# Kernel tuning notes

Hardware: AMD Instinct MI355X
Metric: run time of the kernel (lower is better)

The kernel has to match this reference:

```python
import jax, jax.numpy as jnp
import numpy as np

N = 50000   # nodes
E = 1000000 # edges
D = 64      # input_dim
H = 64      # hidden dim (both hidden layers)
O = 16      # output_dim
G = 512     # number of graphs in the batch


def setup_inputs() -> dict:
    key = jax.random.key(0)
    ks = jax.random.split(key, 12)
    s = 0.05
    x = jax.random.normal(ks[0], (N, D), dtype=jnp.float32)
    edge_index = jax.random.randint(ks[1], (2, E), 0, N, dtype=jnp.int32)
    batch = jnp.sort(jax.random.randint(ks[2], (N,), 0, G, dtype=jnp.int32))
    # SAGEConv layer 1: lin_l (neighbor aggregate, with bias), lin_r (root, no bias)
    Wl1 = jax.random.normal(ks[3], (D, H), dtype=jnp.float32) * s
    Wr1 = jax.random.normal(ks[4], (D, H), dtype=jnp.float32) * s
    b1 = jnp.zeros((H,), dtype=jnp.float32)
    # SAGEConv layer 2
    Wl2 = jax.random.normal(ks[5], (H, H), dtype=jnp.float32) * s
    Wr2 = jax.random.normal(ks[6], (H, H), dtype=jnp.float32) * s
    b2 = jnp.zeros((H,), dtype=jnp.float32)
    # final Linear head
    Wo = jax.random.normal(ks[7], (H, O), dtype=jnp.float32) * s
    bo = jnp.zeros((O,), dtype=jnp.float32)
    return {"x": x, "edge_index": edge_index, "batch": batch,
            "Wl1": Wl1, "Wr1": Wr1, "b1": b1,
            "Wl2": Wl2, "Wr2": Wr2, "b2": b2,
            "Wo": Wo, "bo": bo}


def reference(x, edge_index, batch, Wl1, Wr1, b1, Wl2, Wr2, b2, Wo, bo):
    src, dst = edge_index[0], edge_index[1]  # source_to_target message flow

    def sage(h, Wl, Wr, b):
        # aggr='add': sum messages x_j from src into dst, then
        # out = lin_l(aggr) + lin_r(h)   (PyG SAGEConv, bias on lin_l)
        agg = jax.ops.segment_sum(h[src], dst, num_segments=N)  # [N, d]
        return agg @ Wl + h @ Wr + b

    h = jax.nn.relu(sage(x, Wl1, Wr1, b1))
    h = jax.nn.relu(sage(h, Wl2, Wr2, b2))
    g = jax.ops.segment_sum(h, batch, num_segments=G)  # global_add_pool -> [G, H]
    # dropout is identity in eval mode
    return g @ Wo + bo  # [G, O]
```

## Files before the change

kernel.cpp:

```cpp
#include <hip/hip_runtime.h>


namespace {
constexpr int NN = 50000;
constexpr int NE = 1000000;
constexpr int NG = 512;
constexpr int NO = 16;
constexpr int KB = 98;
constexpr int BCAP = 16000;
constexpr int EPT = 8;
constexpr int EPB = 256 * EPT;
constexpr int SBLK = (NE + EPB - 1) / EPB;
constexpr int SEDGE = 12288;
constexpr int CVT_BLK = (NN * 64 / 8 + 255) / 256;
constexpr int WP_BLK = 64;
}

typedef __attribute__((ext_vector_type(8))) short bf16x8;
typedef __attribute__((ext_vector_type(4))) float f32x4;

__device__ __forceinline__ unsigned short f2bf(float f) {
  unsigned u = __float_as_uint(f);
  u += 0x7FFFu + ((u >> 16) & 1u);
  return (unsigned short)(u >> 16);
}

__global__ __launch_bounds__(256) void prep_all(
    const float* __restrict__ x, unsigned short* __restrict__ x_bf,
    const float* __restrict__ Wl1, const float* __restrict__ Wr1,
    const float* __restrict__ Wl2, const float* __restrict__ Wr2,
    unsigned short* __restrict__ Wt1, unsigned short* __restrict__ Wt2,
    const int* __restrict__ ei, int* __restrict__ bcount,
    unsigned int* __restrict__ ebuf) {
  __shared__ unsigned int stage[EPB];
  __shared__ int cnt[128];
  __shared__ int lbase[128];
  __shared__ int cur[128];
  __shared__ int gbase[128];
  __shared__ int total_sh;
  int b = blockIdx.x;
  int t = threadIdx.x;

  if (b < CVT_BLK) {
    int i = b * 256 + t;
    if (i >= NN * 8) return;
    const float4* p = reinterpret_cast<const float4*>(x) + (size_t)i * 2;
    float4 a = p[0], bb = p[1];
    uint4 u;
    u.x = (unsigned)f2bf(a.x) | ((unsigned)f2bf(a.y) << 16);
    u.y = (unsigned)f2bf(a.z) | ((unsigned)f2bf(a.w) << 16);
    u.z = (unsigned)f2bf(bb.x) | ((unsigned)f2bf(bb.y) << 16);
    u.w = (unsigned)f2bf(bb.z) | ((unsigned)f2bf(bb.w) << 16);
    reinterpret_cast<uint4*>(x_bf)[i] = u;
    return;
  }
  if (b < CVT_BLK + WP_BLK) {
    int id = (b - CVT_BLK) * 256 + t;
    int half = id >> 13;
    int e = id & 8191;
    int nrow = e >> 7;
    int kk = e & 127;
    const float* Wl = half ? Wl2 : Wl1;
    const float* Wr = half ? Wr2 : Wr1;
    unsigned short* Wt = half ? Wt2 : Wt1;
    float v = (kk < 64) ? Wl[kk * 64 + nrow] : Wr[(kk - 64) * 64 + nrow];
    Wt[nrow * 128 + kk] = f2bf(v);
    return;
  }
  int sb = b - (CVT_BLK + WP_BLK);
  if (t < 128) cnt[t] = 0;
  __syncthreads();
  int e0 = sb * EPB;
  unsigned int pk[EPT];
#pragma unroll
  for (int i = 0; i < EPT; ++i) {
    int e = e0 + i * 256 + t;
    if (e < NE) {
      unsigned int src = (unsigned int)ei[e];
      unsigned int dst = (unsigned int)ei[NE + e];
      pk[i] = (dst << 16) | src;
      atomicAdd(&cnt[dst >> 9], 1);
    } else {
      pk[i] = 0xFFFFFFFFu;
    }
  }
  __syncthreads();
  int deg = (t < 128) ? cnt[t] : 0;
  for (int off = 1; off < 128; off <<= 1) {
    int u = (t >= off && t < 128) ? cnt[t - off] : 0;
    __syncthreads();
    if (t < 128) cnt[t] += u;
    __syncthreads();
  }
  if (t < 128) {
    int excl = cnt[t] - deg;
    lbase[t] = excl;
    cur[t] = excl;
    if (t < KB) gbase[t] = t * BCAP + atomicAdd(&bcount[t], deg);
    if (t == 127) total_sh = cnt[127];
  }
  __syncthreads();
#pragma unroll
  for (int i = 0; i < EPT; ++i) {
    if (pk[i] != 0xFFFFFFFFu) {
      int bb2 = pk[i] >> 25;
      int s = atomicAdd(&cur[bb2], 1);
      stage[s] = pk[i];
    }
  }
  __syncthreads();
  int total = total_sh;
  for (int s = t; s < total; s += 256) {
    unsigned int p = stage[s];
    int bb2 = p >> 25;
    ebuf[gbase[bb2] + (s - lbase[bb2])] = p;
  }
}

__global__ __launch_bounds__(512) void bucket_sort(
    const unsigned int* __restrict__ ebuf, const int* __restrict__ bcount,
    unsigned int* __restrict__ meta, unsigned short* __restrict__ col) {
  __shared__ unsigned int se[SEDGE];
  __shared__ int cnt[512];
  __shared__ int cur[512];
  int b = blockIdx.x;
  int t = threadIdx.x;
  int n = bcount[b];
  const unsigned int* eb = ebuf + (size_t)b * BCAP;
  cnt[t] = 0;
  __syncthreads();
  for (int j = t; j < n; j += 512) {
    unsigned int p = eb[j];
    if (j < SEDGE) se[j] = p;
    atomicAdd(&cnt[(p >> 16) & 511], 1);
  }
  __syncthreads();
  int deg = cnt[t];
  for (int off = 1; off < 512; off <<= 1) {
    int u = (t >= off) ? cnt[t - off] : 0;
    __syncthreads();
    cnt[t] += u;
    __syncthreads();
  }
  int excl = cnt[t] - deg;
  cur[t] = excl;
  int node = (b << 9) + t;
  if (node < NN) {
    meta[node] = ((unsigned)(b * BCAP + excl) << 11) | (unsigned)deg;
  }
  __syncthreads();
  unsigned short* cb = col + (size_t)b * BCAP;
  for (int j = t; j < n; j += 512) {
    unsigned int p = (j < SEDGE) ? se[j] : eb[j];
    int d = (p >> 16) & 511;
    int pos = atomicAdd(&cur[d], 1);
    cb[pos] = (unsigned short)(p & 0xFFFFu);
  }
}

template <bool POOL>
__global__ __launch_bounds__(256) void sage_fused(
    const unsigned short* __restrict__ feat,
    const unsigned int* __restrict__ meta,
    const unsigned short* __restrict__ col,
    const unsigned short* __restrict__ Wt, const float* __restrict__ bias,
    unsigned short* __restrict__ out, const int* __restrict__ batch,
    float* __restrict__ pooled) {
  __shared__ __align__(16) unsigned short tile[2][16][72];
  __shared__ float psm[POOL ? 2 : 1][16][64];
  int tid = threadIdx.x;
  int wave = tid >> 6;
  int lane = tid & 63;
  int grp = wave >> 1;
  int wv = wave & 1;
  long base = ((long)blockIdx.x * 2 + grp) * 16;

  {
    int h = lane >> 3;
    int o = lane & 7;
    long row = base + wv * 8 + h;
    int beg = 0, deg = 0;
    if (row < NN) {
      unsigned int md = meta[row];
      beg = (int)(md >> 11);
      deg = (int)(md & 2047u);
    }
    const uint4* fb = reinterpret_cast<const uint4*>(feat);
    float a0 = 0.f, a1 = 0.f, a2 = 0.f, a3 = 0.f;
    float a4 = 0.f, a5 = 0.f, a6 = 0.f, a7 = 0.f;
    for (int j = 0; j < deg; ++j) {
      int s = col[beg + j];
      uint4 u = fb[(size_t)s * 8 + o];
      a0 += __uint_as_float(u.x << 16);
      a1 += __uint_as_float(u.x & 0xFFFF0000u);
      a2 += __uint_as_float(u.y << 16);
      a3 += __uint_as_float(u.y & 0xFFFF0000u);
      a4 += __uint_as_float(u.z << 16);
      a5 += __uint_as_float(u.z & 0xFFFF0000u);
      a6 += __uint_as_float(u.w << 16);
      a7 += __uint_as_float(u.w & 0xFFFF0000u);
    }
    uint4 pk;
    pk.x = (unsigned)f2bf(a0) | ((unsigned)f2bf(a1) << 16);
    pk.y = (unsigned)f2bf(a2) | ((unsigned)f2bf(a3) << 16);
    pk.z = (unsigned)f2bf(a4) | ((unsigned)f2bf(a5) << 16);
    pk.w = (unsigned)f2bf(a6) | ((unsigned)f2bf(a7) << 16);
    *reinterpret_cast<uint4*>(&tile[grp][wv * 8 + h][o * 8]) = pk;
  }
  __syncthreads();

  int m = lane & 15;
  int q = lane >> 4;
  bool active = (base < NN);
  f32x4 acc[2];
  if (active) {
    long rowm = base + m;
    if (rowm >= NN) rowm = NN - 1;
    bf16x8 af[4];
    af[0] = *reinterpret_cast<const bf16x8*>(&tile[grp][m][q * 8]);
    af[1] = *reinterpret_cast<const bf16x8*>(&tile[grp][m][32 + q * 8]);
    const unsigned short* hrow = feat + rowm * 64;
    af[2] = *(const bf16x8*)(hrow + q * 8);
    af[3] = *(const bf16x8*)(hrow + 32 + q * 8);

#pragma unroll
    for (int tt = 0; tt < 2; ++tt) {
      int t = wv * 2 + tt;
      float bv = bias[t * 16 + m];
      acc[tt][0] = bv;
      acc[tt][1] = bv;
      acc[tt][2] = bv;
      acc[tt][3] = bv;
      const unsigned short* wrow = Wt + (size_t)(t * 16 + m) * 128 + q * 8;
#pragma unroll
      for (int s = 0; s < 4; ++s) {
        bf16x8 bfm = *(const bf16x8*)(wrow + s * 32);
        acc[tt] = __builtin_amdgcn_mfma_f32_16x16x32_bf16(af[s], bfm, acc[tt],
                                                          0, 0, 0);
      }
    }

    if (POOL) {
#pragma unroll
      for (int r = 0; r < 4; ++r) {
#pragma unroll
        for (int tt = 0; tt < 2; ++tt) {
          psm[grp][q * 4 + r][(wv * 2 + tt) * 16 + m] = fmaxf(acc[tt][r], 0.f);
        }
      }
    } else {
#pragma unroll
      for (int r = 0; r < 4; ++r) {
        long rowc = base + q * 4 + r;
        if (rowc < NN) {
          unsigned short* orow = out + rowc * 64;
#pragma unroll
          for (int tt = 0; tt < 2; ++tt) {
            orow[(wv * 2 + tt) * 16 + m] = f2bf(fmaxf(acc[tt][r], 0.f));
          }
        }
      }
    }
  }

  if (POOL) {
    __syncthreads();
    if (tid < 128) {
      int g2 = tid >> 6;
      int c = tid & 63;
      long tbase = ((long)blockIdx.x * 2 + g2) * 16;
      if (tbase < NN) {
        float run = 0.f;
        int g = batch[tbase];
        for (int i = 0; i < 16; ++i) {
          long rowi = tbase + i;
          if (rowi >= NN) break;
          int gi = batch[rowi];
          if (gi != g) {
            atomicAdd(&pooled[(size_t)g * 64 + c], run);
            run = 0.f;
            g = gi;
          }
          run += psm[g2][i][c];
        }
        atomicAdd(&pooled[(size_t)g * 64 + c], run);
      }
    }
  }
}

__global__ __launch_bounds__(256) void head_kernel(
    const float* __restrict__ pooled, const float* __restrict__ Wo,
    const float* __restrict__ bo, float* __restrict__ out) {
  int id = blockIdx.x * 256 + threadIdx.x;
  if (id >= NG * NO) return;
  int g = id >> 4, o = id & 15;
  float acc = bo[o];
  const float* p = pooled + (size_t)g * 64;
#pragma unroll
  for (int k = 0; k < 64; ++k) acc += p[k] * Wo[k * 16 + o];
  out[id] = acc;
}

extern "C" void kernel_launch(void* const* d_in, const int* in_sizes, int n_in,
                              void* d_out, int out_size, void* d_ws,
                              size_t ws_size, hipStream_t stream) {
  const float* x = (const float*)d_in[0];
  const int* ei = (const int*)d_in[1];
  const int* batch = (const int*)d_in[2];
  const float* Wl1 = (const float*)d_in[3];
  const float* Wr1 = (const float*)d_in[4];
  const float* b1 = (const float*)d_in[5];
  const float* Wl2 = (const float*)d_in[6];
  const float* Wr2 = (const float*)d_in[7];
  const float* b2 = (const float*)d_in[8];
  const float* Wo = (const float*)d_in[9];
  const float* bo = (const float*)d_in[10];
  float* out = (float*)d_out;

  unsigned short* x_bf = (unsigned short*)d_ws;
  unsigned short* h1_bf = x_bf + (size_t)NN * 64;
  unsigned short* col = h1_bf + (size_t)NN * 64;
  unsigned short* Wt1 = col + (size_t)KB * BCAP;
  unsigned short* Wt2 = Wt1 + 64 * 128;
  unsigned int* ebuf = (unsigned int*)(Wt2 + 64 * 128);
  unsigned int* meta = ebuf + (size_t)KB * BCAP;
  int* bcount = (int*)(meta + NN);
  float* pooled = (float*)(bcount + KB);

  hipMemsetAsync(bcount, 0, KB * sizeof(int) + (size_t)NG * 64 * sizeof(float),
                 stream);

  const int fused_blocks = (NN + 31) / 32;

  prep_all<<<CVT_BLK + WP_BLK + SBLK, 256, 0, stream>>>(
      x, x_bf, Wl1, Wr1, Wl2, Wr2, Wt1, Wt2, ei, bcount, ebuf);

  bucket_sort<<<KB, 512, 0, stream>>>(ebuf, bcount, meta, col);

  sage_fused<false><<<fused_blocks, 256, 0, stream>>>(
      x_bf, meta, col, Wt1, b1, h1_bf, batch, pooled);

  sage_fused<true><<<fused_blocks, 256, 0, stream>>>(
      h1_bf, meta, col, Wt2, b2, nullptr, batch, pooled);

  head_kernel<<<(NG * NO + 255) / 256, 256, 0, stream>>>(pooled, Wo, bo, out);
}
```

Before: 181.8 us.

## Reorder nodes by in-degree within each graph to balance gather loop divergence

Adds a perm_build kernel that, per graph segment of the sorted batch array, counting-sorts nodes by in-degree into a permutation. Both SAGE layers then process nodes in permuted order, so the 8 nodes sharing a wavefront have similar degree and the per-lane gather loop diverges less. Pooling still works because the permutation stays inside each graph's contiguous node range. The cost is an extra kernel launch plus indirect reads of perm and scattered output writes, and neighbouring output rows are no longer contiguous.

Measured after the change: 191.6 us. 5.4% more time.

```diff
diff --git a/kernel.cpp b/kernel.cpp
--- a/kernel.cpp
+++ b/kernel.cpp
@@ -158,11 +158,57 @@
   }
 }
 
+__global__ __launch_bounds__(256) void perm_build(
+    const int* __restrict__ batch, const unsigned int* __restrict__ meta,
+    int* __restrict__ perm) {
+  __shared__ int hist[256];
+  __shared__ int cur[256];
+  __shared__ int bounds[2];
+  int g = blockIdx.x;
+  int t = threadIdx.x;
+  if (t < 2) {
+    int target = g + t;
+    int lo = 0, hi = NN;
+    while (lo < hi) {
+      int mid = (lo + hi) >> 1;
+      if (batch[mid] < target)
+        lo = mid + 1;
+      else
+        hi = mid;
+    }
+    bounds[t] = lo;
+  }
+  hist[t] = 0;
+  __syncthreads();
+  int beg = bounds[0], n = bounds[1] - bounds[0];
+  for (int j = t; j < n; j += 256) {
+    int d = (int)(meta[beg + j] & 2047u);
+    atomicAdd(&hist[d < 255 ? d : 255], 1);
+  }
+  __syncthreads();
+  int v = hist[t];
+  for (int off = 1; off < 256; off <<= 1) {
+    int u = (t >= off) ? hist[t - off] : 0;
+    __syncthreads();
+    hist[t] += u;
+    __syncthreads();
+  }
+  cur[t] = hist[t] - v;
+  __syncthreads();
+  for (int j = t; j < n; j += 256) {
+    int node = beg + j;
+    int d = (int)(meta[node] & 2047u);
+    if (d > 255) d = 255;
+    int pos = atomicAdd(&cur[d], 1);
+    perm[beg + pos] = node;
+  }
+}
+
 template <bool POOL>
 __global__ __launch_bounds__(256) void sage_fused(
     const unsigned short* __restrict__ feat,
     const unsigned int* __restrict__ meta,
-    const unsigned short* __restrict__ col,
+    const unsigned short* __restrict__ col, const int* __restrict__ perm,
     const unsigned short* __restrict__ Wt, const float* __restrict__ bias,
     unsigned short* __restrict__ out, const int* __restrict__ batch,
     float* __restrict__ pooled) {
@@ -178,13 +224,12 @@
   {
     int h = lane >> 3;
     int o = lane & 7;
-    long row = base + wv * 8 + h;
-    int beg = 0, deg = 0;
-    if (row < NN) {
-      unsigned int md = meta[row];
-      beg = (int)(md >> 11);
-      deg = (int)(md & 2047u);
-    }
+    long pidx = base + wv * 8 + h;
+    if (pidx >= NN) pidx = NN - 1;
+    int row = perm[pidx];
+    unsigned int md = meta[row];
+    int beg = (int)(md >> 11);
+    int deg = (int)(md & 2047u);
     const uint4* fb = reinterpret_cast<const uint4*>(feat);
     float a0 = 0.f, a1 = 0.f, a2 = 0.f, a3 = 0.f;
     float a4 = 0.f, a5 = 0.f, a6 = 0.f, a7 = 0.f;
@@ -214,12 +259,13 @@
   bool active = (base < NN);
   f32x4 acc[2];
   if (active) {
-    long rowm = base + m;
-    if (rowm >= NN) rowm = NN - 1;
+    long pm = base + m;
+    if (pm >= NN) pm = NN - 1;
+    int rowm = perm[pm];
     bf16x8 af[4];
     af[0] = *reinterpret_cast<const bf16x8*>(&tile[grp][m][q * 8]);
     af[1] = *reinterpret_cast<const bf16x8*>(&tile[grp][m][32 + q * 8]);
-    const unsigned short* hrow = feat + rowm * 64;
+    const unsigned short* hrow = feat + (size_t)rowm * 64;
     af[2] = *(const bf16x8*)(hrow + q * 8);
     af[3] = *(const bf16x8*)(hrow + 32 + q * 8);
 
@@ -251,9 +297,9 @@
     } else {
 #pragma unroll
       for (int r = 0; r < 4; ++r) {
-        long rowc = base + q * 4 + r;
-        if (rowc < NN) {
-          unsigned short* orow = out + rowc * 64;
+        long rc = base + q * 4 + r;
+        if (rc < NN) {
+          unsigned short* orow = out + (size_t)perm[rc] * 64;
 #pragma unroll
           for (int tt = 0; tt < 2; ++tt) {
             orow[(wv * 2 + tt) * 16 + m] = f2bf(fmaxf(acc[tt][r], 0.f));
@@ -271,11 +317,11 @@
       long tbase = ((long)blockIdx.x * 2 + g2) * 16;
       if (tbase < NN) {
         float run = 0.f;
-        int g = batch[tbase];
+        int g = batch[perm[tbase]];
         for (int i = 0; i < 16; ++i) {
-          long rowi = tbase + i;
-          if (rowi >= NN) break;
-          int gi = batch[rowi];
+          long pi = tbase + i;
+          if (pi >= NN) break;
+          int gi = batch[perm[pi]];
           if (gi != g) {
             atomicAdd(&pooled[(size_t)g * 64 + c], run);
             run = 0.f;
@@ -325,7 +371,8 @@
   unsigned short* Wt2 = Wt1 + 64 * 128;
   unsigned int* ebuf = (unsigned int*)(Wt2 + 64 * 128);
   unsigned int* meta = ebuf + (size_t)KB * BCAP;
-  int* bcount = (int*)(meta + NN);
+  int* perm = (int*)(meta + NN);
+  int* bcount = perm + NN;
   float* pooled = (float*)(bcount + KB);
 
   hipMemsetAsync(bcount, 0, KB * sizeof(int) + (size_t)NG * 64 * sizeof(float),
@@ -337,12 +384,13 @@
       x, x_bf, Wl1, Wr1, Wl2, Wr2, Wt1, Wt2, ei, bcount, ebuf);
 
   bucket_sort<<<KB, 512, 0, stream>>>(ebuf, bcount, meta, col);
+  perm_build<<<NG, 256, 0, stream>>>(batch, meta, perm);
 
   sage_fused<false><<<fused_blocks, 256, 0, stream>>>(
-      x_bf, meta, col, Wt1, b1, h1_bf, batch, pooled);
+      x_bf, meta, col, perm, Wt1, b1, h1_bf, batch, pooled);
 
   sage_fused<true><<<fused_blocks, 256, 0, stream>>>(
-      h1_bf, meta, col, Wt2, b2, nullptr, batch, pooled);
+      h1_bf, meta, col, perm, Wt2, b2, nullptr, batch, pooled);
 
   head_kernel<<<(NG * NO + 255) / 256, 256, 0, stream>>>(pooled, Wo, bo, out);
 }
```
